# Performance work log

Measured on AMD Instinct MI355X. Metric: run time of the kernel, lower is better.

Reference implementation:

```python
import jax, jax.numpy as jnp
import numpy as np

B, N, D = 16, 1024, 16  # graphs, nodes, embedding_dim


def setup_inputs() -> dict:
    key = jax.random.key(0)
    ks = jax.random.split(key, 13)
    s = 0.05  # small weight scale to keep exp(alpha) well-behaved
    return {
        "X": jax.random.normal(ks[0], (B, N, D), dtype=jnp.float32),
        "init_param": jax.random.normal(ks[1], (2,), dtype=jnp.float32) * s,
        "Wq": jax.random.normal(ks[2], (D - 1, D, D), dtype=jnp.float32) * s,
        "bq": jax.random.normal(ks[3], (D - 1, D), dtype=jnp.float32) * s,
        "Wk": jax.random.normal(ks[4], (D - 1, D, D), dtype=jnp.float32) * s,
        "bk": jax.random.normal(ks[5], (D - 1, D), dtype=jnp.float32) * s,
        "Wv": jax.random.normal(ks[6], (D - 1, D, D), dtype=jnp.float32) * s,
        "bv": jax.random.normal(ks[7], (D - 1, D), dtype=jnp.float32) * s,
        "Wo": jax.random.normal(ks[8], (D - 1, D, D), dtype=jnp.float32) * s,
        "bo": jax.random.normal(ks[9], (D - 1, D), dtype=jnp.float32) * s,
        "Wf": jax.random.normal(ks[10], (D - 1, 2, D), dtype=jnp.float32) * s,
        "bf": jax.random.normal(ks[11], (D - 1, 2), dtype=jnp.float32) * s,
    }


def reference(X, init_param, Wq, bq, Wk, bk, Wv, bv, Wo, bo, Wf, bf):
    b, n, d = X.shape
    dt = X.dtype
    Zs = []
    logdet = jnp.zeros((b, n), dt)
    for i in range(d):
        if i == 0:
            mu, alpha = init_param[0], init_param[1]
        else:
            l = i - 1
            Xi = X[:, :, :i]  # [B,N,i] growing ragged slice
            Q = Xi @ Wq[l, :i, :i].T + bq[l, :i]
            K = Xi @ Wk[l, :i, :i].T + bk[l, :i]
            V = Xi @ Wv[l, :i, :i].T + bv[l, :i]
            # SAB/MAB: softmax(QK^T / sqrt(dim_V=i)); num_heads=1
            A = jax.nn.softmax(
                jnp.einsum("bnd,bmd->bnm", Q, K) / jnp.sqrt(jnp.asarray(i, dt)),
                axis=-1,
            )  # [B,N,N]
            O = Q + jnp.einsum("bnm,bmd->bnd", A, V)
            O = O + jax.nn.relu(O @ Wo[l, :i, :i].T + bo[l, :i])
            out = O @ Wf[l, :, :i].T + bf[l]  # [B,N,2]
            mu, alpha = out[..., 0], out[..., 1]
        Zs.append((X[:, :, i] - mu) / jnp.exp(alpha))
        logdet = logdet - alpha
    Z = jnp.stack(Zs, axis=-1)
    return Z, logdet
```

## Files before the change

kernel.cpp:

```cpp
#include <hip/hip_runtime.h>
#include <math.h>

#define Bb 16
#define Nn 1024
#define Dd 16
#define NL 15

typedef __attribute__((ext_vector_type(8))) short short8;
typedef __attribute__((ext_vector_type(16))) float f32x16;
typedef __attribute__((ext_vector_type(4))) unsigned uint4v;

#if __has_builtin(__builtin_amdgcn_exp2f)
#define EXP2(x) __builtin_amdgcn_exp2f(x)
#else
#define EXP2(x) exp2f(x)
#endif

#define PROJ_SZ ((size_t)NL * Bb * 1024 * 16)
#define WS_NEED (3 * PROJ_SZ * 2 + 1088 * 2)

#define VSTR 1040
#define V_OFF 32768
#define ONES_OFF 66048
#define RS_OFF 69632
#define LDS_TOTAL 73728

__device__ __forceinline__ unsigned pack2bf(float a, float b) {
    unsigned ua = __float_as_uint(a) + 0x8000u;
    unsigned ub = __float_as_uint(b) + 0x8000u;
    return (ua >> 16) | (ub & 0xffff0000u);
}
__device__ __forceinline__ unsigned short bf1(float a) {
    return (unsigned short)((__float_as_uint(a) + 0x8000u) >> 16);
}

__device__ __forceinline__ unsigned expperm(float x, float y) {
    unsigned ex = __float_as_uint(EXP2(x));
    unsigned ey = __float_as_uint(EXP2(y));
#if __has_builtin(__builtin_amdgcn_perm)
    return __builtin_amdgcn_perm(ey, ex, 0x07060302);
#else
    return (ex >> 16) | (ey & 0xffff0000u);
#endif
}

__device__ __forceinline__ int vperm(int m) {
    return (m & 3) + ((m & 8) >> 1) + ((m & 4) << 1);
}

__device__ __forceinline__ void project(const float* __restrict__ xrow,
                                        const float* __restrict__ W,
                                        const float* __restrict__ bias,
                                        int i, float* __restrict__ q) {
#pragma unroll
    for (int r = 0; r < 16; r++) q[r] = 0.f;
    for (int c = 0; c < i; c++) {
        float xc = xrow[c];
#pragma unroll
        for (int r = 0; r < 16; r++) q[r] = fmaf(xc, W[r * 16 + c], q[r]);
    }
#pragma unroll
    for (int r = 0; r < 16; r++) q[r] = (r < i) ? (q[r] + bias[r]) : 0.f;
}

__device__ __forceinline__ void load_row16(const float* __restrict__ p, float* __restrict__ x) {
    const float4* xp = (const float4*)p;
    float4 a = xp[0], b = xp[1], c = xp[2], d = xp[3];
    x[0]=a.x; x[1]=a.y; x[2]=a.z; x[3]=a.w;
    x[4]=b.x; x[5]=b.y; x[6]=b.z; x[7]=b.w;
    x[8]=c.x; x[9]=c.y; x[10]=c.z; x[11]=c.w;
    x[12]=d.x; x[13]=d.y; x[14]=d.z; x[15]=d.w;
}

__global__ void gf_init(const float* __restrict__ X, const float* __restrict__ ip,
                        float* __restrict__ out, unsigned short* __restrict__ onesb) {
    int idx = blockIdx.x * blockDim.x + threadIdx.x;
    if (idx >= Bb * Nn) return;
    if (onesb && idx < 1088) onesb[idx] = 0x3F80;
    float mu = ip[0], alpha = ip[1];
    float x0 = X[(size_t)idx * Dd];
    out[(size_t)idx * Dd] = (x0 - mu) * __expf(-alpha);
    out[(size_t)Bb * Nn * Dd + idx] = -alpha;
}

__global__ void gf_proj(const float* __restrict__ X,
                        const float* __restrict__ Wq, const float* __restrict__ bq,
                        const float* __restrict__ Wk, const float* __restrict__ bk,
                        const float* __restrict__ Wv, const float* __restrict__ bv,
                        unsigned short* __restrict__ Kg,
                        unsigned short* __restrict__ Vg,
                        unsigned short* __restrict__ Qg) {
    const int l = blockIdx.x, b = blockIdx.y, i = l + 1;
    const int t = threadIdx.x;
    const size_t lb = (size_t)(l * Bb + b);
    const float qscale = 1.4426950408889634f * rsqrtf((float)i);

    const float* Xb  = X  + (size_t)b * Nn * Dd;
    const float* wq  = Wq + l * 256;  const float* bql = bq + l * 16;
    const float* wk  = Wk + l * 256;  const float* bkl = bk + l * 16;
    const float* wvp = Wv + l * 256;  const float* bvl = bv + l * 16;

    float xr[16]; load_row16(Xb + (size_t)t * Dd, xr);
    float tmp[16];

    project(xr, wk, bkl, i, tmp);
    {
        unsigned u[8];
#pragma unroll
        for (int r = 0; r < 8; r++) u[r] = pack2bf(tmp[2*r], tmp[2*r+1]);
        uint4* kd = (uint4*)(Kg + (lb * 1024 + t) * 16);
        kd[0] = make_uint4(u[0], u[1], u[2], u[3]);
        kd[1] = make_uint4(u[4], u[5], u[6], u[7]);
    }

    project(xr, wvp, bvl, i, tmp);
    {
        unsigned short* vcol = Vg + lb * (16 * 1024) + (t & ~15) + vperm(t & 15);
#pragma unroll
        for (int d = 0; d < 16; d++) vcol[d * 1024] = bf1(tmp[d]);
    }

    project(xr, wq, bql, i, tmp);
    {
        unsigned u[8];
#pragma unroll
        for (int r = 0; r < 8; r++) u[r] = pack2bf(tmp[2*r] * qscale, tmp[2*r+1] * qscale);
        uint4* qd = (uint4*)(Qg + (lb * 1024 + t) * 16);
        qd[0] = make_uint4(u[0], u[1], u[2], u[3]);
        qd[1] = make_uint4(u[4], u[5], u[6], u[7]);
    }
}

__launch_bounds__(256, 5)
__global__ void gf_attn(const float* __restrict__ X,
                        const unsigned short* __restrict__ Kg,
                        const unsigned short* __restrict__ Vg,
                        const unsigned short* __restrict__ Qg,
                        const unsigned short* __restrict__ onesb,
                        const float* __restrict__ Wo, const float* __restrict__ bo,
                        const float* __restrict__ Wf, const float* __restrict__ bf,
                        float* __restrict__ out) {
    __shared__ float Osh[4 * 32 * 17];
    __shared__ float Rsh[4 * 32];

    const int bx = blockIdx.x;
    const int c = bx & 7, k = bx >> 3;
    const int G = c * 30 + (k >> 3);
    const int z = k & 7;
    const int l = G % NL, b = G / NL, i = l + 1;

    const int t = threadIdx.x;
    const int wid = t >> 6, lane = t & 63;
    const int q31 = lane & 31, h = lane >> 5;
    const size_t lb = (size_t)(l * Bb + b);
    const int qbase = z * 128 + wid * 32;

    short8 qf = *(const short8*)(Qg + (lb * 1024 + qbase + q31) * 16 + 8 * h);

    const unsigned short* Kp = Kg + (lb * 1024 + q31) * 16 + 8 * h;
    const unsigned short* Vp = ((q31 < 16) ? (Vg + (lb * 16 + q31) * 1024)
                                           : onesb) + 8 * h;

    const f32x16 zf16 = {};
    f32x16 D = {};

    short8 kf  = *(const short8*)Kp;
    short8 vc0 = *(const short8*)(Vp);
    short8 vc1 = *(const short8*)(Vp + 16);

    for (int lk = 0; lk < Nn; lk += 32) {
        const int kn = (lk + 32) & (Nn - 1);
        short8 kfn = *(const short8*)(Kp + (size_t)kn * 16);
        short8 vn0 = *(const short8*)(Vp + kn);
        short8 vn1 = *(const short8*)(Vp + kn + 16);

        f32x16 s = __builtin_amdgcn_mfma_f32_32x32x16_bf16(kf, qf, zf16, 0, 0, 0);

        {
            uint4v a0 = {expperm(s[0], s[1]), expperm(s[2], s[3]),
                         expperm(s[4], s[5]), expperm(s[6], s[7])};
            D = __builtin_amdgcn_mfma_f32_32x32x16_bf16(
                    __builtin_bit_cast(short8, a0), vc0, D, 0, 0, 0);
        }
        {
            uint4v a1 = {expperm(s[8], s[9]),  expperm(s[10], s[11]),
                         expperm(s[12], s[13]), expperm(s[14], s[15])};
            D = __builtin_amdgcn_mfma_f32_32x32x16_bf16(
                    __builtin_bit_cast(short8, a1), vc1, D, 0, 0, 0);
        }
        kf = kfn; vc0 = vn0; vc1 = vn1;
    }

    float* Ow = Osh + wid * (32 * 17);
    if (q31 < 16) {
#pragma unroll
        for (int r = 0; r < 16; r++) {
            int m = (r & 3) + 8 * (r >> 2) + 4 * h;
            Ow[m * 17 + q31] = D[r];
        }
    }
    if (q31 == 16) {
        float* Rw = Rsh + wid * 32;
#pragma unroll
        for (int r = 0; r < 16; r++) {
            int m = (r & 3) + 8 * (r >> 2) + 4 * h;
            Rw[m] = D[r];
        }
    }
    __syncthreads();

    if (t < 128) {
        const int qn = z * 128 + t;
        const float invq = 0.6931471805599453f * sqrtf((float)i);

        float a[16];
        {
            const uint4* qp = (const uint4*)(Qg + (lb * 1024 + qn) * 16);
            uint4 u0 = qp[0], u1 = qp[1];
            unsigned uw[8] = {u0.x, u0.y, u0.z, u0.w, u1.x, u1.y, u1.z, u1.w};
#pragma unroll
            for (int r = 0; r < 8; r++) {
                a[2*r]     = __uint_as_float(uw[r] << 16) * invq;
                a[2*r + 1] = __uint_as_float(uw[r] & 0xffff0000u) * invq;
            }
        }

        const float* orow = Osh + (t >> 5) * (32 * 17) + (t & 31) * 17;
        const float  inv  = 1.f / Rsh[(t >> 5) * 32 + (t & 31)];
#pragma unroll
        for (int cc = 0; cc < 16; cc++) a[cc] += orow[cc] * inv;

        const float* wo  = Wo + l * 256;  const float* bol = bo + l * 16;
        const float* wf  = Wf + l * 32;   const float* bfl = bf + l * 2;

        float tt[16];
#pragma unroll
        for (int r = 0; r < 16; r++) {
            float acc = bol[r];
#pragma unroll
            for (int cc = 0; cc < 16; cc++) acc = fmaf(a[cc], wo[r * 16 + cc], acc);
            tt[r] = fmaxf(acc, 0.f);
        }
#pragma unroll
        for (int r = 0; r < 16; r++) a[r] += (r < i) ? tt[r] : 0.f;

        float mu = bfl[0], al = bfl[1];
#pragma unroll
        for (int cc = 0; cc < 16; cc++) {
            mu = fmaf(a[cc], wf[cc], mu);
            al = fmaf(a[cc], wf[16 + cc], al);
        }
        const float xi = X[((size_t)b * Nn + qn) * Dd + i];
        out[((size_t)(b * Nn + qn)) * Dd + i] = (xi - mu) * __expf(-al);
        atomicAdd(out + (size_t)Bb * Nn * Dd + b * Nn + qn, -al);
    }
}

__launch_bounds__(1024, 4)
__global__ void gf_fused(const float* __restrict__ X,
                         const float* __restrict__ Wq, const float* __restrict__ bq,
                         const float* __restrict__ Wk, const float* __restrict__ bk,
                         const float* __restrict__ Wv, const float* __restrict__ bv,
                         const float* __restrict__ Wo, const float* __restrict__ bo,
                         const float* __restrict__ Wf, const float* __restrict__ bf,
                         float* __restrict__ out) {
    extern __shared__ char smem[];
    const int l = blockIdx.x, b = blockIdx.y, i = l + 1;
    const int t = threadIdx.x;
    const int wid = t >> 6, lane = t & 63;
    const int q31 = lane & 31, h = lane >> 5;
    const float qscale = 1.4426950408889634f * rsqrtf((float)i);

    unsigned short* Ksh  = (unsigned short*)smem;
    unsigned short* Vsh  = (unsigned short*)(smem + V_OFF);
    unsigned short* Ones = (unsigned short*)(smem + ONES_OFF);

    const float* Xb  = X  + (size_t)b * Nn * Dd;
    const float* wq  = Wq + l * 256;  const float* bql = bq + l * 16;
    const float* wk  = Wk + l * 256;  const float* bkl = bk + l * 16;
    const float* wvp = Wv + l * 256;  const float* bvl = bv + l * 16;
    const float* wo  = Wo + l * 256;  const float* bol = bo + l * 16;
    const float* wf  = Wf + l * 32;   const float* bfl = bf + l * 2;

    unsigned qu[8];
    {
        float xr[16]; load_row16(Xb + (size_t)t * Dd, xr);
        float tmp[16];

        project(xr, wk, bkl, i, tmp);
        {
            unsigned u[8];
#pragma unroll
            for (int r = 0; r < 8; r++) u[r] = pack2bf(tmp[2*r], tmp[2*r+1]);
            uint4* kd = (uint4*)(Ksh + t * 16);
            kd[0] = make_uint4(u[0], u[1], u[2], u[3]);
            kd[1] = make_uint4(u[4], u[5], u[6], u[7]);
        }

        project(xr, wvp, bvl, i, tmp);
        {
            unsigned short* vcol = Vsh + (t & ~15) + vperm(t & 15);
#pragma unroll
            for (int d = 0; d < 16; d++) vcol[d * VSTR] = bf1(tmp[d]);
        }

        Ones[t] = 0x3F80;

        project(xr, wq, bql, i, tmp);
#pragma unroll
        for (int r = 0; r < 8; r++) qu[r] = pack2bf(tmp[2*r] * qscale, tmp[2*r+1] * qscale);
    }
    __syncthreads();

    short8 qf0, qf1;
    {
        unsigned d0[4], d1[4];
#pragma unroll
        for (int j = 0; j < 4; j++) {
            unsigned lo = __shfl(qu[j], q31);
            unsigned hi = __shfl(qu[4 + j], q31);
            d0[j] = h ? hi : lo;
            lo = __shfl(qu[j], 32 + q31);
            hi = __shfl(qu[4 + j], 32 + q31);
            d1[j] = h ? hi : lo;
        }
        uint4v v0 = {d0[0], d0[1], d0[2], d0[3]};
        uint4v v1 = {d1[0], d1[1], d1[2], d1[3]};
        qf0 = __builtin_bit_cast(short8, v0);
        qf1 = __builtin_bit_cast(short8, v1);
    }

    f32x16 zf16 = {};
    f32x16 D0 = {}, D1 = {};

    const unsigned short* Kp = Ksh + (size_t)q31 * 16 + h * 8;
    const unsigned short* Vp = ((q31 < 16) ? (Vsh + (size_t)q31 * VSTR) : Ones) + 8 * h;

    short8 kf  = *(const short8*)Kp;
    short8 vc0 = *(const short8*)(Vp);
    short8 vc1 = *(const short8*)(Vp + 16);

    for (int kb = 0; kb < Nn; kb += 32) {
        const int kn = (kb + 32) & (Nn - 1);
        short8 kfn = *(const short8*)(Kp + (size_t)kn * 16);
        short8 vn0 = *(const short8*)(Vp + kn);
        short8 vn1 = *(const short8*)(Vp + kn + 16);

        f32x16 s0 = __builtin_amdgcn_mfma_f32_32x32x16_bf16(kf, qf0, zf16, 0, 0, 0);
        f32x16 s1 = __builtin_amdgcn_mfma_f32_32x32x16_bf16(kf, qf1, zf16, 0, 0, 0);
        kf = kfn;

        {
            uint4v a0 = {expperm(s0[0], s0[1]), expperm(s0[2], s0[3]),
                         expperm(s0[4], s0[5]), expperm(s0[6], s0[7])};
            D0 = __builtin_amdgcn_mfma_f32_32x32x16_bf16(
                     __builtin_bit_cast(short8, a0), vc0, D0, 0, 0, 0);
            uint4v a1 = {expperm(s1[0], s1[1]), expperm(s1[2], s1[3]),
                         expperm(s1[4], s1[5]), expperm(s1[6], s1[7])};
            D1 = __builtin_amdgcn_mfma_f32_32x32x16_bf16(
                     __builtin_bit_cast(short8, a1), vc0, D1, 0, 0, 0);
        }
        {
            uint4v a0 = {expperm(s0[8], s0[9]),  expperm(s0[10], s0[11]),
                         expperm(s0[12], s0[13]), expperm(s0[14], s0[15])};
            D0 = __builtin_amdgcn_mfma_f32_32x32x16_bf16(
                     __builtin_bit_cast(short8, a0), vc1, D0, 0, 0, 0);
            uint4v a1 = {expperm(s1[8], s1[9]),  expperm(s1[10], s1[11]),
                         expperm(s1[12], s1[13]), expperm(s1[14], s1[15])};
            D1 = __builtin_amdgcn_mfma_f32_32x32x16_bf16(
                     __builtin_bit_cast(short8, a1), vc1, D1, 0, 0, 0);
        }
        vc0 = vn0; vc1 = vn1;
    }

    __syncthreads();

    float* Ow = (float*)smem + wid * (64 * 17);
    if (q31 < 16) {
#pragma unroll
        for (int r = 0; r < 16; r++) {
            int m = (r & 3) + 8 * (r >> 2) + 4 * h;
            Ow[m * 17 + q31]        = D0[r];
            Ow[(m + 32) * 17 + q31] = D1[r];
        }
    }
    float* Rw = (float*)(smem + RS_OFF) + wid * 64;
    if (q31 == 16) {
#pragma unroll
        for (int r = 0; r < 16; r++) {
            int m = (r & 3) + 8 * (r >> 2) + 4 * h;
            Rw[m]      = D0[r];
            Rw[32 + m] = D1[r];
        }
    }

    {
        const float invq = 0.6931471805599453f * sqrtf((float)i);

        float a[16];
#pragma unroll
        for (int r = 0; r < 8; r++) {
            a[2*r]     = __uint_as_float(qu[r] << 16) * invq;
            a[2*r + 1] = __uint_as_float(qu[r] & 0xffff0000u) * invq;
        }

        const float* orow = (const float*)smem + wid * (64 * 17) + lane * 17;
        const float  inv  = 1.f / Rw[lane];
#pragma unroll
        for (int c = 0; c < 16; c++) a[c] += orow[c] * inv;

        float tt[16];
#pragma unroll
        for (int r = 0; r < 16; r++) {
            float acc = bol[r];
#pragma unroll
            for (int c = 0; c < 16; c++) acc = fmaf(a[c], wo[r * 16 + c], acc);
            tt[r] = fmaxf(acc, 0.f);
        }
#pragma unroll
        for (int r = 0; r < 16; r++) a[r] += (r < i) ? tt[r] : 0.f;

        float mu = bfl[0], al = bfl[1];
#pragma unroll
        for (int c = 0; c < 16; c++) {
            mu = fmaf(a[c], wf[c], mu);
            al = fmaf(a[c], wf[16 + c], al);
        }
        const float xi = Xb[(size_t)t * Dd + i];
        out[((size_t)(b * Nn + t)) * Dd + i] = (xi - mu) * __expf(-al);
        atomicAdd(out + (size_t)Bb * Nn * Dd + b * Nn + t, -al);
    }
}

__launch_bounds__(512, 2)
__global__ void gf_layer_fb(const float* __restrict__ X,
                            const float* __restrict__ Wq, const float* __restrict__ bq,
                            const float* __restrict__ Wk, const float* __restrict__ bk,
                            const float* __restrict__ Wv, const float* __restrict__ bv,
                            const float* __restrict__ Wo, const float* __restrict__ bo,
                            const float* __restrict__ Wf, const float* __restrict__ bf,
                            float* __restrict__ out) {
    const int l = blockIdx.x, b = blockIdx.y, i = l + 1, t = threadIdx.x;
    const float rscale = rsqrtf((float)i);
    __shared__ float Ksh[512 * 16];
    __shared__ float Vsh[512 * 16];
    const float* Xb = X + (size_t)b * Nn * Dd;
    const float* wq = Wq + l * 256; const float* wk = Wk + l * 256;
    const float* wv = Wv + l * 256; const float* wo = Wo + l * 256;
    const float* wf = Wf + l * 32;
    const float* bql = bq + l * 16; const float* bkl = bk + l * 16;
    const float* bvl = bv + l * 16; const float* bol = bo + l * 16;
    const float* bfl = bf + l * 2;
    const int n0 = t, n1 = t + 512;
    float q0[16], q1[16], xi0, xi1;
    {
        float xr[16];
        load_row16(Xb + (size_t)n0 * Dd, xr); xi0 = xr[i]; project(xr, wq, bql, i, q0);
        load_row16(Xb + (size_t)n1 * Dd, xr); xi1 = xr[i]; project(xr, wq, bql, i, q1);
    }
    float o0[16], o1[16];
#pragma unroll
    for (int c = 0; c < 16; c++) { o0[c] = 0.f; o1[c] = 0.f; }
    float ls0 = 0.f, ls1 = 0.f;
    for (int ch = 0; ch < 2; ch++) {
        float kr[16], vr[16];
        {
            float kx[16];
            load_row16(Xb + (size_t)(ch * 512 + t) * Dd, kx);
            project(kx, wk, bkl, i, kr);
            project(kx, wv, bvl, i, vr);
        }
        __syncthreads();
#pragma unroll
        for (int j = 0; j < 4; j++) {
            ((float4*)&Ksh[t * 16])[j] = ((float4*)kr)[j];
            ((float4*)&Vsh[t * 16])[j] = ((float4*)vr)[j];
        }
        __syncthreads();
        for (int k = 0; k < 512; k++) {
            float kk[16], vv[16];
#pragma unroll
            for (int j = 0; j < 4; j++) ((float4*)kk)[j] = ((const float4*)&Ksh[k * 16])[j];
            float s0 = 0.f, s1 = 0.f;
#pragma unroll
            for (int c = 0; c < 16; c++) { s0 = fmaf(q0[c], kk[c], s0); s1 = fmaf(q1[c], kk[c], s1); }
            float p0 = __expf(s0 * rscale), p1 = __expf(s1 * rscale);
            ls0 += p0; ls1 += p1;
#pragma unroll
            for (int j = 0; j < 4; j++) ((float4*)vv)[j] = ((const float4*)&Vsh[k * 16])[j];
#pragma unroll
            for (int c = 0; c < 16; c++) { o0[c] = fmaf(p0, vv[c], o0[c]); o1[c] = fmaf(p1, vv[c], o1[c]); }
        }
        __syncthreads();
    }
    float* logdet = out + (size_t)Bb * Nn * Dd;
#pragma unroll
    for (int rowsel = 0; rowsel < 2; rowsel++) {
        const float* qr = rowsel ? q1 : q0; const float* orr = rowsel ? o1 : o0;
        float lsum = rowsel ? ls1 : ls0; float xin = rowsel ? xi1 : xi0;
        int n = rowsel ? n1 : n0;
        float a[16]; float inv = 1.f / lsum;
#pragma unroll
        for (int c = 0; c < 16; c++) a[c] = qr[c] + orr[c] * inv;
        float tt[16];
#pragma unroll
        for (int r = 0; r < 16; r++) {
            float acc = bol[r];
#pragma unroll
            for (int c = 0; c < 16; c++) acc = fmaf(a[c], wo[r * 16 + c], acc);
            tt[r] = fmaxf(acc, 0.f);
        }
#pragma unroll
        for (int r = 0; r < 16; r++) a[r] += (r < i) ? tt[r] : 0.f;
        float mu = bfl[0], al = bfl[1];
#pragma unroll
        for (int c = 0; c < 16; c++) { mu = fmaf(a[c], wf[c], mu); al = fmaf(a[c], wf[16 + c], al); }
        out[((size_t)(b * Nn + n)) * Dd + i] = (xin - mu) * __expf(-al);
        atomicAdd(logdet + b * Nn + n, -al);
    }
}

extern "C" void kernel_launch(void* const* d_in, const int* in_sizes, int n_in,
                              void* d_out, int out_size, void* d_ws, size_t ws_size,
                              hipStream_t stream) {
    const float* X  = (const float*)d_in[0];
    const float* ip = (const float*)d_in[1];
    const float* Wq = (const float*)d_in[2];
    const float* bq = (const float*)d_in[3];
    const float* Wk = (const float*)d_in[4];
    const float* bk = (const float*)d_in[5];
    const float* Wv = (const float*)d_in[6];
    const float* bv = (const float*)d_in[7];
    const float* Wo = (const float*)d_in[8];
    const float* bo = (const float*)d_in[9];
    const float* Wf = (const float*)d_in[10];
    const float* bf = (const float*)d_in[11];
    float* out = (float*)d_out;

    if (ws_size >= WS_NEED && d_ws != nullptr) {
        unsigned short* Kg    = (unsigned short*)d_ws;
        unsigned short* Vg    = Kg + PROJ_SZ;
        unsigned short* Qg    = Vg + PROJ_SZ;
        unsigned short* onesb = Qg + PROJ_SZ;

        gf_init<<<(Bb * Nn + 255) / 256, 256, 0, stream>>>(X, ip, out, onesb);
        gf_proj<<<dim3(NL, Bb), 1024, 0, stream>>>(X, Wq, bq, Wk, bk, Wv, bv,
                                                   Kg, Vg, Qg);
        gf_attn<<<NL * Bb * 8, 256, 0, stream>>>(X, Kg, Vg, Qg, onesb,
                                                 Wo, bo, Wf, bf, out);
        return;
    }

    gf_init<<<(Bb * Nn + 255) / 256, 256, 0, stream>>>(X, ip, out, nullptr);

    hipError_t e = hipFuncSetAttribute((const void*)gf_fused,
                                       hipFuncAttributeMaxDynamicSharedMemorySize,
                                       LDS_TOTAL);
    if (e == hipSuccess) {
        gf_fused<<<dim3(NL, Bb), 1024, LDS_TOTAL, stream>>>(
            X, Wq, bq, Wk, bk, Wv, bv, Wo, bo, Wf, bf, out);
    } else {
        gf_layer_fb<<<dim3(NL, Bb), 512, 0, stream>>>(
            X, Wq, bq, Wk, bk, Wv, bv, Wo, bo, Wf, bf, out);
    }
}
```

Measured before the change: 166.3 us.

## Software-pipeline QK MFMA one tile ahead and stage V transpose through LDS

The attention loop now computes the next tile's QK^T scores while the exp and PV MFMAs of the current tile run. K and V fragments are prefetched two tiles ahead, which lets the score MFMA latency overlap with the exp work. Launch bounds are lowered from 5 to 4 waves per SIMD to make room for the extra live registers. The projection kernel also stages the transposed V through shared memory so it can be written to global memory with coalesced 16-byte stores instead of scattered 2-byte stores.

```diff
diff --git a/kernel.cpp b/kernel.cpp
--- a/kernel.cpp
+++ b/kernel.cpp
@@ -90,6 +90,7 @@
                         unsigned short* __restrict__ Kg,
                         unsigned short* __restrict__ Vg,
                         unsigned short* __restrict__ Qg) {
+    __shared__ unsigned short Vt[16 * 1040];
     const int l = blockIdx.x, b = blockIdx.y, i = l + 1;
     const int t = threadIdx.x;
     const size_t lb = (size_t)(l * Bb + b);
@@ -115,9 +116,9 @@
 
     project(xr, wvp, bvl, i, tmp);
     {
-        unsigned short* vcol = Vg + lb * (16 * 1024) + (t & ~15) + vperm(t & 15);
-#pragma unroll
-        for (int d = 0; d < 16; d++) vcol[d * 1024] = bf1(tmp[d]);
+        const int col = (t & ~15) + vperm(t & 15);
+#pragma unroll
+        for (int d = 0; d < 16; d++) Vt[d * 1040 + col] = bf1(tmp[d]);
     }
 
     project(xr, wq, bql, i, tmp);
@@ -129,9 +130,18 @@
         qd[0] = make_uint4(u[0], u[1], u[2], u[3]);
         qd[1] = make_uint4(u[4], u[5], u[6], u[7]);
     }
-}
-
-__launch_bounds__(256, 5)
+
+    __syncthreads();
+    {
+        const int d = t >> 6, seg = t & 63;
+        const uint4* src = (const uint4*)(Vt + d * 1040 + seg * 16);
+        uint4* dst = (uint4*)(Vg + lb * (16 * 1024) + d * 1024 + seg * 16);
+        dst[0] = src[0];
+        dst[1] = src[1];
+    }
+}
+
+__launch_bounds__(256, 4)
 __global__ void gf_attn(const float* __restrict__ X,
                         const unsigned short* __restrict__ Kg,
                         const unsigned short* __restrict__ Vg,
@@ -164,31 +174,43 @@
     const f32x16 zf16 = {};
     f32x16 D = {};
 
-    short8 kf  = *(const short8*)Kp;
-    short8 vc0 = *(const short8*)(Vp);
-    short8 vc1 = *(const short8*)(Vp + 16);
+    short8 kf_in, vc0, vc1, vn0, vn1;
+    f32x16 s_cur;
+    {
+        short8 k0 = *(const short8*)Kp;
+        vc0 = *(const short8*)(Vp);
+        vc1 = *(const short8*)(Vp + 16);
+        s_cur = __builtin_amdgcn_mfma_f32_32x32x16_bf16(k0, qf, zf16, 0, 0, 0);
+        kf_in = *(const short8*)(Kp + 32 * 16);
+        vn0 = *(const short8*)(Vp + 32);
+        vn1 = *(const short8*)(Vp + 48);
+    }
 
     for (int lk = 0; lk < Nn; lk += 32) {
-        const int kn = (lk + 32) & (Nn - 1);
-        short8 kfn = *(const short8*)(Kp + (size_t)kn * 16);
-        short8 vn0 = *(const short8*)(Vp + kn);
-        short8 vn1 = *(const short8*)(Vp + kn + 16);
-
-        f32x16 s = __builtin_amdgcn_mfma_f32_32x32x16_bf16(kf, qf, zf16, 0, 0, 0);
-
-        {
-            uint4v a0 = {expperm(s[0], s[1]), expperm(s[2], s[3]),
-                         expperm(s[4], s[5]), expperm(s[6], s[7])};
+        const int kn = (lk + 64) & (Nn - 1);
+        short8 kf2 = *(const short8*)(Kp + (size_t)kn * 16);
+        short8 w0  = *(const short8*)(Vp + kn);
+        short8 w1  = *(const short8*)(Vp + kn + 16);
+
+        f32x16 s_nxt = __builtin_amdgcn_mfma_f32_32x32x16_bf16(kf_in, qf, zf16, 0, 0, 0);
+
+        {
+            uint4v a0 = {expperm(s_cur[0], s_cur[1]), expperm(s_cur[2], s_cur[3]),
+                         expperm(s_cur[4], s_cur[5]), expperm(s_cur[6], s_cur[7])};
             D = __builtin_amdgcn_mfma_f32_32x32x16_bf16(
                     __builtin_bit_cast(short8, a0), vc0, D, 0, 0, 0);
         }
         {
-            uint4v a1 = {expperm(s[8], s[9]),  expperm(s[10], s[11]),
-                         expperm(s[12], s[13]), expperm(s[14], s[15])};
+            uint4v a1 = {expperm(s_cur[8], s_cur[9]),  expperm(s_cur[10], s_cur[11]),
+                         expperm(s_cur[12], s_cur[13]), expperm(s_cur[14], s_cur[15])};
             D = __builtin_amdgcn_mfma_f32_32x32x16_bf16(
                     __builtin_bit_cast(short8, a1), vc1, D, 0, 0, 0);
         }
-        kf = kfn; vc0 = vn0; vc1 = vn1;
+
+        s_cur = s_nxt;
+        kf_in = kf2;
+        vc0 = vn0; vc1 = vn1;
+        vn0 = w0;  vn1 = w1;
     }
 
     float* Ow = Osh + wid * (32 * 17);
```

Measured after the change: 164.2 us. Within noise of the previous version (-1.2%).
